# Kernel optimization log

Measured on AMD Instinct MI355X. Metric: run time of the kernel, lower is better.

## Reference

```python
import jax, jax.numpy as jnp
import numpy as np

EPS = 0.05
ITERS = 10


def setup_inputs() -> dict:
    key = jax.random.key(0)
    k1, k2, k3 = jax.random.split(key, 3)
    x = jax.random.normal(k1, (32, 768, 32, 32), jnp.float32)          # [B,C,H,W]
    conv_w = jax.random.normal(k2, (384, 768), jnp.float32) * 0.02     # 1x1 conv kernel [D,C]
    conv_b = jnp.zeros((384,), jnp.float32)
    v = jax.random.normal(k3, (64, 384), jnp.float32)                  # cluster codebook [K,D]
    return {"x": x, "conv_w": conv_w, "conv_b": conv_b, "v": v}


def log_sinkhorn_iterations(Z, log_mu, log_nu, iters):
    # Z: [B,M,N]; log_mu: [B,M]; log_nu: [B,N]
    u0 = jnp.zeros_like(log_mu)
    v0 = jnp.zeros_like(log_nu)

    def step(carry, _):
        u, v = carry
        u = log_mu - jax.nn.logsumexp(Z + v[:, None, :], axis=2)
        v = log_nu - jax.nn.logsumexp(Z + u[:, :, None], axis=1)
        return (u, v), None

    (u, v), _ = jax.lax.scan(step, (u0, v0), None, length=iters)
    return Z + u[:, :, None] + v[:, None, :]


def log_optimal_transport(scores, eps, iters):
    b, m, n = scores.shape
    norm = -jnp.log(jnp.asarray(float(m + n), scores.dtype))
    log_mu = jnp.full((b, m), norm, scores.dtype)
    log_nu = jnp.full((b, n), norm, scores.dtype)
    Z = log_sinkhorn_iterations(scores / eps, log_mu, log_nu, iters)
    return jnp.exp(Z - norm)


def reference(x, conv_w, conv_b, v):
    b, c, h, w = x.shape
    d = conv_w.shape[0]
    # 1x1 conv projection, then flatten spatial and move channels last: [B, HW, D]
    x_proj = jnp.einsum('bchw,dc->bhwd', x, conv_w).reshape(b, h * w, d) + conv_b
    # l2_normalize tokens
    xn = x_proj / jnp.maximum(jnp.linalg.norm(x_proj, axis=-1, keepdims=True), 1e-12)
    # normalized cluster codebook (torch does this under no_grad + in-place copy)
    clusters = v / jnp.maximum(jnp.linalg.norm(v, axis=-1, keepdims=True), 1e-12)  # [K,D]
    # cluster scores: [B, HW, K]
    scores = jnp.einsum('bnd,kd->bnk', xn, clusters)
    # OT on transposed scores [B,K,HW], transpose weights back to [B,HW,K]
    weights = jnp.transpose(
        log_optimal_transport(jnp.transpose(scores, (0, 2, 1)), EPS, ITERS), (0, 2, 1))
    # v_tilde = (x^T @ weights)^T : [B, K, D]
    v_tilde = jnp.einsum('bnd,bnk->bkd', xn, weights)
    return (v_tilde, x_proj)
```

## Files before the change

kernel.cpp:

```cpp
#include <hip/hip_runtime.h>
#include <math.h>

#define BB 32
#define CC 768
#define HWN 1024
#define DD 384
#define KK 64
#define EPSI 20.0f
#define NORMC (-6.9920964f)
#define NITERS 10

typedef __bf16 bf16;
typedef bf16 bf16x8 __attribute__((ext_vector_type(8)));
typedef bf16 bf16x4 __attribute__((ext_vector_type(4)));
typedef float f32x4 __attribute__((ext_vector_type(4)));
typedef _Float16 f16;
typedef f16 f16x2 __attribute__((ext_vector_type(2)));
typedef f16 f16x4 __attribute__((ext_vector_type(4)));

__device__ __forceinline__ float wave_sum(float v){
  #pragma unroll
  for (int off = 32; off; off >>= 1) v += __shfl_xor(v, off, 64);
  return v;
}
__device__ __forceinline__ float wave_max(float v){
  #pragma unroll
  for (int off = 32; off; off >>= 1) v = fmaxf(v, __shfl_xor(v, off, 64));
  return v;
}

__device__ __forceinline__ void async16(const bf16* g, bf16* l){
  __builtin_amdgcn_global_load_lds((const __attribute__((address_space(1))) unsigned int*)g,
                                   (__attribute__((address_space(3))) unsigned int*)l,
                                   16, 0, 0);
}

__global__ __launch_bounds__(256) void k0_clusters(const float* __restrict__ vin,
                                                   bf16* __restrict__ clusb){
  int w = threadIdx.x >> 6, l = threadIdx.x & 63;
  int k = blockIdx.x * 4 + w;
  float s = 0.f;
  #pragma unroll
  for (int i = 0; i < 6; i++){ float x = vin[k*DD + l + 64*i]; s += x*x; }
  s = wave_sum(s);
  float scale = 1.f / fmaxf(sqrtf(s), 1e-12f);
  #pragma unroll
  for (int i = 0; i < 6; i++) clusb[k*DD + l + 64*i] = (bf16)(vin[k*DD + l + 64*i] * scale);
}

__global__ __launch_bounds__(256) void k_wconv(const float* __restrict__ w,
                                               bf16* __restrict__ wb){
  int i = (blockIdx.x * 256 + threadIdx.x) * 4;
  float4 v = *(const float4*)&w[i];
  bf16x4 o;
  o[0] = (bf16)v.x; o[1] = (bf16)v.y; o[2] = (bf16)v.z; o[3] = (bf16)v.w;
  *(bf16x4*)&wb[i] = o;
}

__global__ __launch_bounds__(512) void k_gemm(const bf16* __restrict__ Wb,
                                              const float* __restrict__ X,
                                              const float* __restrict__ bias,
                                              float* __restrict__ xp,
                                              bf16* __restrict__ xnb){
  __shared__ bf16  Wl[384][4][8];
  __shared__ float Xf[128 * 36];
  __shared__ float part[4][128];
  __shared__ float rn_l[128];
  int b  = blockIdx.y;
  int n0 = blockIdx.x * 128;
  int t = threadIdx.x, wv = t >> 6, l = t & 63;
  int l15 = l & 15, quad = l >> 4;
  int wn = wv >> 2, wm = wv & 3;
  const float* Xg = X + (size_t)b * CC * HWN;

  int rbase = wv*16 + (l >> 2);
  int kq8   = (l & 3) * 8;
  const bf16* gW = Wb + (size_t)rbase * CC + kq8;
  bf16* lW = &Wl[0][0][0] + wv * 512;

  int q = t & 31, h = t >> 5;
  int n4 = q * 4, c2 = h * 2;
  int sthr = (q ^ (q >> 2)) & 3;
  int coff = (((c2 >> 3) ^ sthr) << 3) + (c2 & 7);

  f32x4 acc[4][6];
  const f32x4 zero = {0.f, 0.f, 0.f, 0.f};
  #pragma unroll
  for (int i = 0; i < 4; i++)
    #pragma unroll
    for (int j = 0; j < 6; j++) acc[i][j] = zero;

  int a_ = l15 >> 2;

  for (int c0 = 0; c0 < CC; c0 += 32){
    const float* xr = Xg + (size_t)(c0 + c2) * HWN + n0 + n4;
    float4 v0 = *(const float4*)xr;
    float4 v1 = *(const float4*)(xr + HWN);
    {
      float2 w0; w0.x = v0.x; w0.y = v1.x;
      float2 w1; w1.x = v0.y; w1.y = v1.y;
      float2 w2; w2.x = v0.z; w2.y = v1.z;
      float2 w3; w3.x = v0.w; w3.y = v1.w;
      *(float2*)&Xf[(n4+0)*36 + coff] = w0;
      *(float2*)&Xf[(n4+1)*36 + coff] = w1;
      *(float2*)&Xf[(n4+2)*36 + coff] = w2;
      *(float2*)&Xf[(n4+3)*36 + coff] = w3;
    }
    async16(gW + c0,                  lW);
    async16(gW + c0 + (size_t)128*CC, lW + 4096);
    async16(gW + c0 + (size_t)256*CC, lW + 8192);
    __syncthreads();

    bf16x8 xf[4], wf[6];
    #pragma unroll
    for (int i = 0; i < 4; i++){
      int nloc = wn*64 + i*16 + l15;
      int s = (a_ ^ (wn*4 + i)) & 3;
      int blk = quad ^ s;
      const float4 f0 = *(const float4*)&Xf[nloc*36 + blk*8];
      const float4 f1 = *(const float4*)&Xf[nloc*36 + blk*8 + 4];
      bf16x8 xv;
      xv[0] = (bf16)f0.x; xv[1] = (bf16)f0.y; xv[2] = (bf16)f0.z; xv[3] = (bf16)f0.w;
      xv[4] = (bf16)f1.x; xv[5] = (bf16)f1.y; xv[6] = (bf16)f1.z; xv[7] = (bf16)f1.w;
      xf[i] = xv;
    }
    #pragma unroll
    for (int j = 0; j < 6; j++)
      wf[j] = *(const bf16x8*)&Wl[wm*96 + j*16 + l15][quad][0];
    #pragma unroll
    for (int i = 0; i < 4; i++)
      #pragma unroll
      for (int j = 0; j < 6; j++)
        acc[i][j] = __builtin_amdgcn_mfma_f32_16x16x32_bf16(xf[i], wf[j], acc[i][j], 0, 0, 0);
    __syncthreads();
  }

  float bb[6];
  #pragma unroll
  for (int j = 0; j < 6; j++) bb[j] = bias[wm*96 + j*16 + l15];

  #pragma unroll
  for (int i = 0; i < 4; i++){
    #pragma unroll
    for (int r = 0; r < 4; r++){
      float s = 0.f;
      #pragma unroll
      for (int j = 0; j < 6; j++){ float v = acc[i][j][r] + bb[j]; s = fmaf(v, v, s); }
      s += __shfl_xor(s, 1, 64); s += __shfl_xor(s, 2, 64);
      s += __shfl_xor(s, 4, 64); s += __shfl_xor(s, 8, 64);
      if (l15 == 0) part[wm][wn*64 + i*16 + quad*4 + r] = s;
    }
  }
  __syncthreads();
  if (t < 128){
    float tot = part[0][t] + part[1][t] + part[2][t] + part[3][t];
    rn_l[t] = 1.f / fmaxf(sqrtf(tot), 1e-12f);
  }
  __syncthreads();

  #pragma unroll
  for (int i = 0; i < 4; i++){
    #pragma unroll
    for (int r = 0; r < 4; r++){
      int nloc = wn*64 + i*16 + quad*4 + r;
      float rv = rn_l[nloc];
      float* orow = xp  + ((size_t)b * HWN + n0 + nloc) * DD;
      bf16*  xrow = xnb + ((size_t)b * HWN + n0 + nloc) * DD;
      #pragma unroll
      for (int j = 0; j < 6; j++){
        int m = wm*96 + j*16 + l15;
        float val = acc[i][j][r] + bb[j];
        orow[m] = val;
        xrow[m] = (bf16)(val * rv);
      }
    }
  }
}

__global__ __launch_bounds__(256) void k_xpt2(const bf16* __restrict__ xnb,
                                              bf16* __restrict__ xpt){
  __shared__ bf16 S[64][72];
  int b  = blockIdx.z;
  int d0 = blockIdx.y * 64;
  int n0 = blockIdx.x * 64;
  const bf16* src = xnb + ((size_t)b * HWN + n0) * DD + d0;
  int t = threadIdx.x;
  int r = t >> 3, c8 = (t & 7) * 8;
  #pragma unroll
  for (int it = 0; it < 2; it++){
    bf16x8 v = *(const bf16x8*)&src[(size_t)(r + it*32) * DD + c8];
    *(bf16x8*)&S[r + it*32][c8] = v;
  }
  __syncthreads();
  int d = t >> 2, c0 = (t & 3) * 16;
  bf16* orow = xpt + ((size_t)b * DD + d0 + d) * HWN + n0 + c0;
  bf16x8 o0, o1;
  #pragma unroll
  for (int jj = 0; jj < 8; jj++) o0[jj] = S[c0 + jj][d];
  #pragma unroll
  for (int jj = 0; jj < 8; jj++) o1[jj] = S[c0 + 8 + jj][d];
  *(bf16x8*)&orow[0] = o0;
  *(bf16x8*)&orow[8] = o1;
}

__global__ __launch_bounds__(256) void k3_scores(const bf16* __restrict__ clusb,
                                                 const bf16* __restrict__ xnb,
                                                 float* __restrict__ Z){
  __shared__ bf16 Al[64][4][8];
  __shared__ bf16 Bl[128][4][8];
  int b = blockIdx.y, n0 = blockIdx.x * 128;
  const bf16* Xb = xnb + (size_t)b * HWN * DD;
  int t = threadIdx.x, wv = t >> 6, l = t & 63;
  int l15 = l & 15, quad = l >> 4;

  int rbase = wv*16 + (l >> 2);
  int kq8   = (l & 3) * 8;
  const bf16* gA = clusb + (size_t)rbase * DD + kq8;
  const bf16* gB = Xb + (size_t)(n0 + rbase) * DD + kq8;
  bf16* lA = &Al[0][0][0] + wv * 512;
  bf16* lB = &Bl[0][0][0] + wv * 512;

  f32x4 acc[4][2];
  const f32x4 zero = {0.f, 0.f, 0.f, 0.f};
  #pragma unroll
  for (int i = 0; i < 4; i++){ acc[i][0] = zero; acc[i][1] = zero; }

  for (int d0 = 0; d0 < DD; d0 += 32){
    async16(gA + d0, lA);
    async16(gB + d0,                 lB);
    async16(gB + d0 + (size_t)64*DD, lB + 2048);
    __syncthreads();
    bf16x8 af[4], bf[2];
    #pragma unroll
    for (int i = 0; i < 4; i++)
      af[i] = *(const bf16x8*)&Al[i*16 + l15][quad][0];
    #pragma unroll
    for (int j = 0; j < 2; j++)
      bf[j] = *(const bf16x8*)&Bl[wv*32 + j*16 + l15][quad][0];
    #pragma unroll
    for (int i = 0; i < 4; i++)
      #pragma unroll
      for (int j = 0; j < 2; j++)
        acc[i][j] = __builtin_amdgcn_mfma_f32_16x16x32_bf16(af[i], bf[j], acc[i][j], 0, 0, 0);
    __syncthreads();
  }
  #pragma unroll
  for (int i = 0; i < 4; i++){
    #pragma unroll
    for (int j = 0; j < 2; j++){
      int n = n0 + wv*32 + j*16 + l15;
      #pragma unroll
      for (int r = 0; r < 4; r++){
        int k = i*16 + quad*4 + r;
        Z[((size_t)b*KK + k)*HWN + n] = acc[i][j][r] * EPSI;
      }
    }
  }
}

__global__ __launch_bounds__(1024) void k4_sinkhorn(const float* __restrict__ Z,
                                                    float* __restrict__ U,
                                                    float* __restrict__ V){
  __shared__ f16  E[64][1024];
  __shared__ float evf[1024];
  __shared__ float eu[64];
  __shared__ float rmax[64];
  __shared__ float u_l[64];
  __shared__ float v_l[1024];
  __shared__ float sp[2][1024];
  int b = blockIdx.x;
  const float* Zb = Z + (size_t)b * KK * HWN;
  int t = threadIdx.x, w = t >> 6, l = t & 63;

  #pragma unroll
  for (int rr = 0; rr < 4; rr++){
    int r = w*4 + rr;
    float4 z[4];
    float mx = -INFINITY;
    #pragma unroll
    for (int j = 0; j < 4; j++){
      z[j] = *(const float4*)&Zb[(size_t)r*HWN + 4*l + 256*j];
      mx = fmaxf(mx, fmaxf(fmaxf(z[j].x, z[j].y), fmaxf(z[j].z, z[j].w)));
    }
    mx = wave_max(mx);
    if (l == 0) rmax[r] = mx;
    #pragma unroll
    for (int j = 0; j < 4; j++){
      f16x4 e4;
      e4[0] = (f16)__expf(z[j].x - mx); e4[1] = (f16)__expf(z[j].y - mx);
      e4[2] = (f16)__expf(z[j].z - mx); e4[3] = (f16)__expf(z[j].w - mx);
      *(f16x4*)&E[r][4*l + 256*j] = e4;
    }
  }
  evf[t] = 1.f;
  v_l[t] = 0.f;
  __syncthreads();

  for (int it = 0; it < NITERS; it++){
    float evx[16];
    #pragma unroll
    for (int j = 0; j < 8; j++){
      float2 e2 = *(const float2*)&evf[2*(l + 64*j)];
      evx[2*j] = e2.x; evx[2*j+1] = e2.y;
    }
    float us[4];
    #pragma unroll
    for (int rr = 0; rr < 4; rr++){
      int r = w*4 + rr;
      float s = 0.f;
      #pragma unroll
      for (int j = 0; j < 8; j++){
        f16x2 e2 = *(const f16x2*)&E[r][2*(l + 64*j)];
        s = fmaf((float)e2[0], evx[2*j],   s);
        s = fmaf((float)e2[1], evx[2*j+1], s);
      }
      us[rr] = wave_sum(s);
    }
    if (l == 0){
      #pragma unroll
      for (int rr = 0; rr < 4; rr++){
        int r = w*4 + rr;
        u_l[r] = NORMC - rmax[r] - __logf(us[rr]);
        eu[r]  = __expf(NORMC) / us[rr];
      }
    }
    __syncthreads();
    {
      int p = t & 511, h = t >> 9;
      float sx = 0.f, sy = 0.f;
      #pragma unroll
      for (int mq = 0; mq < 8; mq++){
        float4 eu4 = *(const float4*)&eu[h*32 + mq*4];
        const float euv[4] = {eu4.x, eu4.y, eu4.z, eu4.w};
        #pragma unroll
        for (int i = 0; i < 4; i++){
          f16x2 e2 = *(const f16x2*)&E[h*32 + mq*4 + i][2*p];
          sx = fmaf((float)e2[0], euv[i], sx);
          sy = fmaf((float)e2[1], euv[i], sy);
        }
      }
      float2 o; o.x = sx; o.y = sy;
      *(float2*)&sp[h][2*p] = o;
    }
    __syncthreads();
    if (t < 512){
      int p = t;
      float2 a = *(const float2*)&sp[0][2*p];
      float2 c = *(const float2*)&sp[1][2*p];
      float vx = NORMC - __logf(a.x + c.x);
      float vy = NORMC - __logf(a.y + c.y);
      v_l[2*p]   = vx;
      v_l[2*p+1] = vy;
      float2 ee; ee.x = __expf(vx); ee.y = __expf(vy);
      *(float2*)&evf[2*p] = ee;
    }
    __syncthreads();
  }
  V[b*HWN + t] = v_l[t];
  if (t < 64) U[b*KK + t] = u_l[t];
}

__global__ __launch_bounds__(256) void k5_mfma(const float* __restrict__ Z,
                                               const float* __restrict__ U,
                                               const float* __restrict__ V,
                                               const bf16* __restrict__ XpT,
                                               float* __restrict__ out){
  __shared__ bf16 El[64][40];
  __shared__ bf16 Xl[384][40];
  int b  = blockIdx.y;
  int nsb = blockIdx.x * 128;
  const float* Zb = Z + (size_t)b * KK * HWN;
  const bf16*  Xb = XpT + (size_t)b * DD * HWN;
  const float* Vb = V + (size_t)b * HWN;
  int t = threadIdx.x, wv = t >> 6, l = t & 63;
  int l15 = l & 15, quad = l >> 4;
  int er = t >> 2, ec0 = (t & 3) * 8;
  float ur = U[b*KK + er];

  f32x4 acc[4][6];
  const f32x4 zero = {0.f, 0.f, 0.f, 0.f};
  #pragma unroll
  for (int i = 0; i < 4; i++)
    #pragma unroll
    for (int j = 0; j < 6; j++) acc[i][j] = zero;

  for (int st = 0; st < 4; st++){
    int n0 = nsb + st*32;
    {
      float4 z0 = *(const float4*)&Zb[(size_t)er*HWN + n0 + ec0];
      float4 z1 = *(const float4*)&Zb[(size_t)er*HWN + n0 + ec0 + 4];
      float4 v0 = *(const float4*)&Vb[n0 + ec0];
      float4 v1 = *(const float4*)&Vb[n0 + ec0 + 4];
      bf16x8 e;
      e[0] = (bf16)__expf(z0.x + ur + v0.x - NORMC);
      e[1] = (bf16)__expf(z0.y + ur + v0.y - NORMC);
      e[2] = (bf16)__expf(z0.z + ur + v0.z - NORMC);
      e[3] = (bf16)__expf(z0.w + ur + v0.w - NORMC);
      e[4] = (bf16)__expf(z1.x + ur + v1.x - NORMC);
      e[5] = (bf16)__expf(z1.y + ur + v1.y - NORMC);
      e[6] = (bf16)__expf(z1.z + ur + v1.z - NORMC);
      e[7] = (bf16)__expf(z1.w + ur + v1.w - NORMC);
      *(bf16x8*)&El[er][ec0] = e;
    }
    #pragma unroll
    for (int ii = 0; ii < 6; ii++){
      int chunk = t + 256*ii;
      int d = chunk >> 2, cb = (chunk & 3) * 8;
      bf16x8 xv = *(const bf16x8*)&Xb[(size_t)d*HWN + n0 + cb];
      *(bf16x8*)&Xl[d][cb] = xv;
    }
    __syncthreads();
    bf16x8 af[4], bfr[6];
    #pragma unroll
    for (int i = 0; i < 4; i++)
      af[i] = *(const bf16x8*)&El[i*16 + l15][quad*8];
    #pragma unroll
    for (int j = 0; j < 6; j++)
      bfr[j] = *(const bf16x8*)&Xl[wv*96 + j*16 + l15][quad*8];
    #pragma unroll
    for (int i = 0; i < 4; i++)
      #pragma unroll
      for (int j = 0; j < 6; j++)
        acc[i][j] = __builtin_amdgcn_mfma_f32_16x16x32_bf16(af[i], bfr[j], acc[i][j], 0, 0, 0);
    __syncthreads();
  }

  float* ob = out + (size_t)b * KK * DD;
  #pragma unroll
  for (int i = 0; i < 4; i++){
    int kbase = i*16 + quad*4;
    #pragma unroll
    for (int j = 0; j < 6; j++){
      int d = wv*96 + j*16 + l15;
      #pragma unroll
      for (int r = 0; r < 4; r++)
        unsafeAtomicAdd(&ob[(size_t)(kbase + r)*DD + d], acc[i][j][r]);
    }
  }
}

extern "C" void kernel_launch(void* const* d_in, const int* in_sizes, int n_in,
                              void* d_out, int out_size, void* d_ws, size_t ws_size,
                              hipStream_t stream) {
  const float* x      = (const float*)d_in[0];
  const float* conv_w = (const float*)d_in[1];
  const float* conv_b = (const float*)d_in[2];
  const float* vcode  = (const float*)d_in[3];
  float* out = (float*)d_out;
  float* vt_out = out;
  float* xp_out = out + 786432;

  bf16* xnb   = (bf16*)d_ws;
  bf16* XpT   = xnb + (size_t)BB * HWN * DD;
  bf16* Wb    = XpT + (size_t)BB * HWN * DD;
  bf16* clusb = Wb + (size_t)DD * CC;
  float* Zbuf = (float*)(clusb + 24576);
  float* Ubuf = Zbuf + 2097152;
  float* Vbuf = Ubuf + 2048;

  hipMemsetAsync(vt_out, 0, (size_t)786432 * sizeof(float), stream);
  k0_clusters<<<16, 256, 0, stream>>>(vcode, clusb);
  k_wconv<<<288, 256, 0, stream>>>(conv_w, Wb);
  k_gemm<<<dim3(8, 32), 512, 0, stream>>>(Wb, x, conv_b, xp_out, xnb);
  k_xpt2<<<dim3(16, 6, 32), 256, 0, stream>>>(xnb, XpT);
  k3_scores<<<dim3(8, 32), 256, 0, stream>>>(clusb, xnb, Zbuf);
  k4_sinkhorn<<<32, 1024, 0, stream>>>(Zbuf, Ubuf, Vbuf);
  k5_mfma<<<dim3(8, 32), 256, 0, stream>>>(Zbuf, Ubuf, Vbuf, XpT, vt_out);
}
```

Measured before the change: 295.9 us.

## Halve GEMM N-tile to 64, prefetch X into registers, new LDS swizzle

The projection GEMM now covers 64 spatial positions per block instead of 128, which doubles the grid to 512 blocks so more of the GPU's CUs get work. The next X slab is loaded into registers while the current step's MFMAs run, and the trailing barrier moves to the top of the loop. The X tile uses an unpadded 32-float row with an XOR swizzle to avoid LDS bank conflicts. In exchange, each block reloads the full 384x768 weight matrix, so the weights are read from L2 twice as often.

```diff
diff --git a/kernel.cpp b/kernel.cpp
--- a/kernel.cpp
+++ b/kernel.cpp
@@ -63,76 +63,64 @@
                                               float* __restrict__ xp,
                                               bf16* __restrict__ xnb){
   __shared__ bf16  Wl[384][4][8];
-  __shared__ float Xf[128 * 36];
-  __shared__ float part[4][128];
-  __shared__ float rn_l[128];
+  __shared__ float Xf[64 * 32];
+  __shared__ float part[4][64];
+  __shared__ float rn_l[64];
   int b  = blockIdx.y;
-  int n0 = blockIdx.x * 128;
+  int n0 = blockIdx.x * 64;
   int t = threadIdx.x, wv = t >> 6, l = t & 63;
   int l15 = l & 15, quad = l >> 4;
   int wn = wv >> 2, wm = wv & 3;
   const float* Xg = X + (size_t)b * CC * HWN;
 
-  int rbase = wv*16 + (l >> 2);
-  int kq8   = (l & 3) * 8;
-  const bf16* gW = Wb + (size_t)rbase * CC + kq8;
+  const bf16* gW = Wb + (size_t)(t >> 2) * CC + (t & 3) * 8;
   bf16* lW = &Wl[0][0][0] + wv * 512;
 
-  int q = t & 31, h = t >> 5;
-  int n4 = q * 4, c2 = h * 2;
-  int sthr = (q ^ (q >> 2)) & 3;
-  int coff = (((c2 >> 3) ^ sthr) << 3) + (c2 & 7);
-
-  f32x4 acc[4][6];
+  int cs = t >> 4, n4 = (t & 15) * 4;
+  const float* gX = Xg + n0 + n4;
+  int pw = (t & 15) >> 1;
+  int physw = ((((cs >> 2) ^ pw) & 7) << 2) | (cs & 3);
+  float* xw = &Xf[n4 * 32 + physw];
+
+  f32x4 acc[2][6];
   const f32x4 zero = {0.f, 0.f, 0.f, 0.f};
   #pragma unroll
-  for (int i = 0; i < 4; i++)
+  for (int i = 0; i < 2; i++)
     #pragma unroll
     for (int j = 0; j < 6; j++) acc[i][j] = zero;
 
-  int a_ = l15 >> 2;
+  float4 xv = *(const float4*)(gX + (size_t)cs * HWN);
 
   for (int c0 = 0; c0 < CC; c0 += 32){
-    const float* xr = Xg + (size_t)(c0 + c2) * HWN + n0 + n4;
-    float4 v0 = *(const float4*)xr;
-    float4 v1 = *(const float4*)(xr + HWN);
-    {
-      float2 w0; w0.x = v0.x; w0.y = v1.x;
-      float2 w1; w1.x = v0.y; w1.y = v1.y;
-      float2 w2; w2.x = v0.z; w2.y = v1.z;
-      float2 w3; w3.x = v0.w; w3.y = v1.w;
-      *(float2*)&Xf[(n4+0)*36 + coff] = w0;
-      *(float2*)&Xf[(n4+1)*36 + coff] = w1;
-      *(float2*)&Xf[(n4+2)*36 + coff] = w2;
-      *(float2*)&Xf[(n4+3)*36 + coff] = w3;
-    }
+    __syncthreads();
+    xw[0] = xv.x; xw[32] = xv.y; xw[64] = xv.z; xw[96] = xv.w;
     async16(gW + c0,                  lW);
     async16(gW + c0 + (size_t)128*CC, lW + 4096);
     async16(gW + c0 + (size_t)256*CC, lW + 8192);
     __syncthreads();
-
-    bf16x8 xf[4], wf[6];
-    #pragma unroll
-    for (int i = 0; i < 4; i++){
-      int nloc = wn*64 + i*16 + l15;
-      int s = (a_ ^ (wn*4 + i)) & 3;
-      int blk = quad ^ s;
-      const float4 f0 = *(const float4*)&Xf[nloc*36 + blk*8];
-      const float4 f1 = *(const float4*)&Xf[nloc*36 + blk*8 + 4];
-      bf16x8 xv;
-      xv[0] = (bf16)f0.x; xv[1] = (bf16)f0.y; xv[2] = (bf16)f0.z; xv[3] = (bf16)f0.w;
-      xv[4] = (bf16)f1.x; xv[5] = (bf16)f1.y; xv[6] = (bf16)f1.z; xv[7] = (bf16)f1.w;
-      xf[i] = xv;
+    if (c0 + 32 < CC)
+      xv = *(const float4*)(gX + (size_t)(c0 + 32 + cs) * HWN);
+
+    bf16x8 xf[2], wf[6];
+    #pragma unroll
+    for (int i = 0; i < 2; i++){
+      int nloc = wn*32 + i*16 + l15;
+      int p = (nloc >> 3) & 7;
+      const float4 f0 = *(const float4*)&Xf[nloc*32 + (((2*quad + 0) ^ p) << 2)];
+      const float4 f1 = *(const float4*)&Xf[nloc*32 + (((2*quad + 1) ^ p) << 2)];
+      bf16x8 c8;
+      c8[0] = (bf16)f0.x; c8[1] = (bf16)f0.y; c8[2] = (bf16)f0.z; c8[3] = (bf16)f0.w;
+      c8[4] = (bf16)f1.x; c8[5] = (bf16)f1.y; c8[6] = (bf16)f1.z; c8[7] = (bf16)f1.w;
+      xf[i] = c8;
     }
     #pragma unroll
     for (int j = 0; j < 6; j++)
       wf[j] = *(const bf16x8*)&Wl[wm*96 + j*16 + l15][quad][0];
     #pragma unroll
-    for (int i = 0; i < 4; i++)
+    for (int i = 0; i < 2; i++)
       #pragma unroll
       for (int j = 0; j < 6; j++)
         acc[i][j] = __builtin_amdgcn_mfma_f32_16x16x32_bf16(xf[i], wf[j], acc[i][j], 0, 0, 0);
-    __syncthreads();
   }
 
   float bb[6];
@@ -140,7 +128,7 @@
   for (int j = 0; j < 6; j++) bb[j] = bias[wm*96 + j*16 + l15];
 
   #pragma unroll
-  for (int i = 0; i < 4; i++){
+  for (int i = 0; i < 2; i++){
     #pragma unroll
     for (int r = 0; r < 4; r++){
       float s = 0.f;
@@ -148,21 +136,21 @@
       for (int j = 0; j < 6; j++){ float v = acc[i][j][r] + bb[j]; s = fmaf(v, v, s); }
       s += __shfl_xor(s, 1, 64); s += __shfl_xor(s, 2, 64);
       s += __shfl_xor(s, 4, 64); s += __shfl_xor(s, 8, 64);
-      if (l15 == 0) part[wm][wn*64 + i*16 + quad*4 + r] = s;
+      if (l15 == 0) part[wm][wn*32 + i*16 + quad*4 + r] = s;
     }
   }
   __syncthreads();
-  if (t < 128){
+  if (t < 64){
     float tot = part[0][t] + part[1][t] + part[2][t] + part[3][t];
     rn_l[t] = 1.f / fmaxf(sqrtf(tot), 1e-12f);
   }
   __syncthreads();
 
   #pragma unroll
-  for (int i = 0; i < 4; i++){
+  for (int i = 0; i < 2; i++){
     #pragma unroll
     for (int r = 0; r < 4; r++){
-      int nloc = wn*64 + i*16 + quad*4 + r;
+      int nloc = wn*32 + i*16 + quad*4 + r;
       float rv = rn_l[nloc];
       float* orow = xp  + ((size_t)b * HWN + n0 + nloc) * DD;
       bf16*  xrow = xnb + ((size_t)b * HWN + n0 + nloc) * DD;
@@ -461,7 +449,7 @@
   hipMemsetAsync(vt_out, 0, (size_t)786432 * sizeof(float), stream);
   k0_clusters<<<16, 256, 0, stream>>>(vcode, clusb);
   k_wconv<<<288, 256, 0, stream>>>(conv_w, Wb);
-  k_gemm<<<dim3(8, 32), 512, 0, stream>>>(Wb, x, conv_b, xp_out, xnb);
+  k_gemm<<<dim3(16, 32), 512, 0, stream>>>(Wb, x, conv_b, xp_out, xnb);
   k_xpt2<<<dim3(16, 6, 32), 256, 0, stream>>>(xnb, XpT);
   k3_scores<<<dim3(8, 32), 256, 0, stream>>>(clusb, xnb, Zbuf);
   k4_sinkhorn<<<32, 1024, 0, stream>>>(Zbuf, Ubuf, Vbuf);
```

Result: faster. 273.9 us (-7.4%).
